# Kernel tuning notes

Hardware: AMD Instinct MI355X
Metric: run time of the kernel (lower is better)

The kernel has to match this reference:

```python
import jax, jax.numpy as jnp
import numpy as np

B, S, D, H = 32, 512, 512, 8  # note: source requires S == D due to swapped shape tuple in multi_head_attention
DK = D // H  # 64
FF = 200     # hard-coded FFN width in source
LN_EPS = 1e-5


def setup_inputs() -> dict:
    key = jax.random.key(0)
    ks = jax.random.split(key, 20)
    s = 0.02
    return {
        "x": jax.random.normal(ks[0], (B, S, D), dtype=jnp.float32),
        # per-head projections, stacked: torch Linear weight shape is [out, in] = [DK, D]
        "Wq": jax.random.normal(ks[1], (H, DK, D), dtype=jnp.float32) * s,
        "bq": jax.random.normal(ks[2], (H, DK), dtype=jnp.float32) * s,
        "Wk": jax.random.normal(ks[3], (H, DK, D), dtype=jnp.float32) * s,
        "bk": jax.random.normal(ks[4], (H, DK), dtype=jnp.float32) * s,
        "Wv": jax.random.normal(ks[5], (H, DK, D), dtype=jnp.float32) * s,
        "bv": jax.random.normal(ks[6], (H, DK), dtype=jnp.float32) * s,
        "Wo": jax.random.normal(ks[7], (D, D), dtype=jnp.float32) * s,
        "bo": jax.random.normal(ks[8], (D,), dtype=jnp.float32) * s,
        "W1": jax.random.normal(ks[9], (FF, D), dtype=jnp.float32) * s,
        "b1": jax.random.normal(ks[10], (FF,), dtype=jnp.float32) * s,
        "W2": jax.random.normal(ks[11], (FF, FF), dtype=jnp.float32) * s,
        "b2": jax.random.normal(ks[12], (FF,), dtype=jnp.float32) * s,
        "W3": jax.random.normal(ks[13], (D, FF), dtype=jnp.float32) * s,
        "b3": jax.random.normal(ks[14], (D,), dtype=jnp.float32) * s,
        # single SHARED LayerNorm over last two dims (S, D)
        "gamma": jnp.ones((S, D), dtype=jnp.float32),
        "beta": jnp.zeros((S, D), dtype=jnp.float32),
    }


def _layernorm2d(y, gamma, beta):
    # torch LayerNorm(normalized_shape=(S, D)): normalize over last two axes, biased variance
    m = jnp.mean(y, axis=(-2, -1), keepdims=True)
    v = jnp.mean(jnp.square(y - m), axis=(-2, -1), keepdims=True)
    return (y - m) * jax.lax.rsqrt(v + LN_EPS) * gamma + beta


def reference(x, Wq, bq, Wk, bk, Wv, bv, Wo, bo, W1, b1, W2, b2, W3, b3, gamma, beta):
    # --- multi-head attention (vectorized over the original per-head Python loop) ---
    q = jnp.einsum('bsd,hkd->bhsk', x, Wq) + bq[None, :, None, :]
    k = jnp.einsum('bsd,hkd->bhsk', x, Wk) + bk[None, :, None, :]
    v = jnp.einsum('bsd,hkd->bhsk', x, Wv) + bv[None, :, None, :]
    scores = jnp.einsum('bhsk,bhtk->bhst', q, k) / jnp.sqrt(jnp.float32(DK))
    attn = jax.nn.softmax(scores, axis=-1)
    heads = jnp.einsum('bhst,bhtk->bhsk', attn, v)          # [B,H,S,DK]
    concat = heads.transpose(0, 2, 1, 3).reshape(B, S, D)    # concat heads along feature dim
    y = jnp.einsum('bsd,ed->bse', concat, Wo) + bo + x       # output proj + residual
    # --- post-attention LayerNorm (shared params) ---
    y = _layernorm2d(y, gamma, beta)
    # --- feed-forward: D -> 200 -> 200 -> D, residual, LayerNorm (same shared LN) ---
    f = jax.nn.relu(jnp.einsum('bsd,fd->bsf', y, W1) + b1)
    f = jax.nn.relu(jnp.einsum('bsf,gf->bsg', f, W2) + b2)
    f = jnp.einsum('bsf,df->bsd', f, W3) + b3
    y = _layernorm2d(f + y, gamma, beta)
    # --- final LayerNorm (same shared LN again) ---
    return _layernorm2d(y, gamma, beta)
```

## Files before the change

kernel.cpp:

```cpp
#include <hip/hip_runtime.h>
#include <hip/hip_bf16.h>
#include <stdint.h>

#define B_  32
#define S_  512
#define D_  512
#define H_  8
#define DK_ 64
#define FF_ 200
#define FFP 256
#define M_  (B_*S_)
#define MSD ((size_t)B_*S_*D_)

typedef __hip_bfloat16 bf16;
typedef __attribute__((ext_vector_type(8))) short short8;
typedef __attribute__((ext_vector_type(4))) float f32x4;
typedef __attribute__((ext_vector_type(4))) unsigned short us4;

__device__ inline float b2f(bf16 v) { return __bfloat162float(v); }
__device__ inline bf16  f2b(float v){ return __float2bfloat16(v); }
__device__ inline unsigned short f2bu(float v) {
  union { bf16 h; unsigned short u; } cv; cv.h = __float2bfloat16(v); return cv.u;
}
__device__ __forceinline__ void async16(const bf16* g, bf16* l) {
  __builtin_amdgcn_global_load_lds((const __attribute__((address_space(1))) void*)g,
                                   (__attribute__((address_space(3))) void*)l, 16, 0, 0);
}

__global__ void detect_kernel(const unsigned short* __restrict__ xu, int* __restrict__ flag) {
  __shared__ int mx[256];
  const int tid = threadIdx.x;
  int m = 0;
  for (int i = tid * 2; i < 8192; i += 512) {
    int e = (xu[i] >> 7) & 0xFF;
    m = m > e ? m : e;
  }
  mx[tid] = m;
  __syncthreads();
  for (int st = 128; st; st >>= 1) {
    if (tid < st) mx[tid] = mx[tid] > mx[tid + st] ? mx[tid] : mx[tid + st];
    __syncthreads();
  }
  if (tid == 0) *flag = (mx[0] >= 0xC0) ? 1 : 0;
}

__global__ void zero_stats(float* stats) { if (threadIdx.x < 192) stats[threadIdx.x] = 0.f; }

__global__ __launch_bounds__(256) void cvt_x8(const void* __restrict__ in, bf16* __restrict__ out,
                                              const int* __restrict__ flag) {
  const bool f32in = (*flag != 0);
  size_t i = ((size_t)blockIdx.x * 256 + threadIdx.x) * 8;
  const size_t stride = (size_t)gridDim.x * 256 * 8;
  for (; i < MSD; i += stride) {
    if (f32in) {
      const float4 a = ((const float4*)in)[i/4];
      const float4 b = ((const float4*)in)[i/4 + 1];
      uint4 o; unsigned short* po = (unsigned short*)&o;
      po[0]=f2bu(a.x); po[1]=f2bu(a.y); po[2]=f2bu(a.z); po[3]=f2bu(a.w);
      po[4]=f2bu(b.x); po[5]=f2bu(b.y); po[6]=f2bu(b.z); po[7]=f2bu(b.w);
      *(uint4*)((unsigned short*)out + i) = o;
    } else {
      *(uint4*)((unsigned short*)out + i) = *(const uint4*)((const unsigned short*)in + i);
    }
  }
}

struct Seg { const void* src; void* dst; int srcRows, srcK, dstK, total; };
struct Segs { Seg s[16]; unsigned int isbf; };

__global__ __launch_bounds__(256) void cvt_all(Segs sg, const int* __restrict__ flag) {
  const bool f32in = (*flag != 0);
  const int seg = blockIdx.x & 15;
  const Seg sd = sg.s[seg];
  const int stride = (gridDim.x >> 4) * 256;
  const bool nopad = (sd.srcK == sd.dstK);
  for (int i = (blockIdx.x >> 4) * 256 + threadIdx.x; i < sd.total; i += stride) {
    int sidx; bool valid;
    if (nopad) { sidx = i; valid = (i < sd.srcRows * sd.srcK); }
    else {
      int r = i / sd.dstK, c = i - r * sd.dstK;
      valid = (r < sd.srcRows) && (c < sd.srcK);
      sidx = r * sd.srcK + c;
    }
    float v = 0.f;
    if (valid) v = f32in ? ((const float*)sd.src)[sidx] : b2f(((const bf16*)sd.src)[sidx]);
    if (sg.isbf & (1u << seg)) ((unsigned short*)sd.dst)[i] = f2bu(v);
    else                       ((float*)sd.dst)[i] = v;
  }
}

template<int MODE, int STATS, typename OUT>
__global__ __launch_bounds__(256) void gemm_mfma(
    const bf16* __restrict__ A, const bf16* __restrict__ W, const float* __restrict__ bias,
    const bf16* __restrict__ R, OUT* __restrict__ C, int M, int N, int K,
    float* __restrict__ stats)
{
  __shared__ bf16 As[128 * 32];
  __shared__ bf16 Bs[128 * 32];
  const int tid  = threadIdx.x;
  const int bm   = blockIdx.x * 128;
  const int bn   = blockIdx.y * 128;
  const int w    = tid >> 6;
  const int lane = tid & 63;
  const int qd   = lane >> 4;
  const int ln   = lane & 15;
  const int wr   = (w >> 1) * 64;
  const int wc   = (w & 1) * 64;

  const int r0 = lane >> 2;
  const int ch = (lane & 3) * 8;
  const bf16* Ag0 = A + (size_t)(bm + w*16 + r0) * K + ch;
  const bf16* Ag1 = Ag0 + (size_t)64 * K;
  const bf16* Bg0 = W + (size_t)(bn + w*16 + r0) * K + ch;
  const bf16* Bg1 = Bg0 + (size_t)64 * K;
  bf16* Al0 = As + w*512 + lane*8;
  bf16* Al1 = Al0 + 2048;
  bf16* Bl0 = Bs + w*512 + lane*8;
  bf16* Bl1 = Bl0 + 2048;

  f32x4 acc[4][4] = {};

  for (int k0 = 0; k0 < K; k0 += 32) {
    async16(Ag0 + k0, Al0);
    async16(Ag1 + k0, Al1);
    async16(Bg0 + k0, Bl0);
    async16(Bg1 + k0, Bl1);
    __syncthreads();

    short8 af[4], bfr[4];
#pragma unroll
    for (int i = 0; i < 4; i++) af[i]  = *(const short8*)(As + (wr + i*16 + ln)*32 + qd*8);
#pragma unroll
    for (int j = 0; j < 4; j++) bfr[j] = *(const short8*)(Bs + (wc + j*16 + ln)*32 + qd*8);
#pragma unroll
    for (int i = 0; i < 4; i++)
#pragma unroll
      for (int j = 0; j < 4; j++)
        acc[i][j] = __builtin_amdgcn_mfma_f32_16x16x32_bf16(af[i], bfr[j], acc[i][j], 0, 0, 0);
    __syncthreads();
  }

  float s_acc = 0.f, ss_acc = 0.f;
#pragma unroll
  for (int i = 0; i < 4; i++) {
#pragma unroll
    for (int j = 0; j < 4; j++) {
      int n = bn + wc + j*16 + ln;
      float bval = bias[n];
#pragma unroll
      for (int rg = 0; rg < 4; rg++) {
        int m = bm + wr + i*16 + qd*4 + rg;
        float val = acc[i][j][rg] + bval;
        if (MODE == 1) val = fmaxf(val, 0.f);
        if (MODE == 2) val += b2f(R[(size_t)m * N + n]);
        if (STATS) { s_acc += val; ss_acc += val * val; }
        if (MODE == 5) {
          int b = m >> 9, s = m & 511, t = n >> 9, nn = n & 511;
          int h = nn >> 6, dk = nn & 63;
          bf16* Cb = (bf16*)C;
          if (t == 2) Cb[2*MSD + ((size_t)((b*H_ + h)*DK_ + dk))*S_ + s] = f2b(val);
          else        Cb[(size_t)t*MSD + ((size_t)((b*H_ + h)*S_ + s))*DK_ + dk] = f2b(val);
        } else {
          if (sizeof(OUT) == 4) ((float*)C)[(size_t)m * N + n] = val;
          else                  ((bf16*)C)[(size_t)m * N + n]  = f2b(val);
        }
      }
    }
  }

  if (STATS) {
    float* red = (float*)As;
    red[tid] = s_acc; red[256 + tid] = ss_acc;
    __syncthreads();
    for (int st = 128; st; st >>= 1) {
      if (tid < st) { red[tid] += red[tid + st]; red[256 + tid] += red[256 + tid + st]; }
      __syncthreads();
    }
    if (tid == 0) {
      int b = bm >> 9;
      atomicAdd(&stats[b*2],     red[0]);
      atomicAdd(&stats[b*2 + 1], red[256]);
    }
  }
}

__global__ __launch_bounds__(1024, 4) void attn_lds(const bf16* __restrict__ q,
    const bf16* __restrict__ k, const bf16* __restrict__ vT, bf16* __restrict__ cat)
{
  __shared__ bf16 Ks[2 * 512 * 32];
  __shared__ bf16 Vs[64 * 520];
  __shared__ bf16 pbuf[16][16][40];

  const int tid  = threadIdx.x;
  const int w    = tid >> 6;
  const int lane = tid & 63;
  const int qd   = lane >> 4;
  const int ln   = lane & 15;
  const int bh   = blockIdx.x;
  const int b    = bh >> 3, h = bh & 7;

  const bf16* kbase = k  + (size_t)bh * S_ * DK_;
  const bf16* vbase = vT + (size_t)bh * DK_ * S_;

  for (int c = tid; c < 4096; c += 1024) {
    int part = c & 3, key = (c >> 2) & 511, ks = c >> 11;
    async16(kbase + key*64 + ks*32 + part*8, Ks + c*8);
  }
  {
    int j = tid & 63;
    for (int dk = tid >> 6; dk < 64; dk += 16) {
      uint4 v = *(const uint4*)(vbase + (size_t)dk*512 + j*8);
      *(uint4*)(Vs + dk*520 + j*8) = v;
    }
  }
  const bf16* qbase = q + (size_t)(bh*S_ + w*32) * DK_;
  short8 bq[2][2];
#pragma unroll
  for (int qt = 0; qt < 2; qt++)
#pragma unroll
    for (int ks = 0; ks < 2; ks++)
      bq[qt][ks] = *(const short8*)(qbase + (size_t)(qt*16 + ln)*DK_ + ks*32 + qd*8);

  __syncthreads();

  bf16 (*pb)[40] = pbuf[w];
  f32x4 o[2][4] = {};
  float l[2] = {0.f, 0.f};

  for (int st = 0; st < 16; st++) {
    short8 ak[2][2];
#pragma unroll
    for (int kt = 0; kt < 2; kt++)
#pragma unroll
      for (int ks = 0; ks < 2; ks++)
        ak[kt][ks] = *(const short8*)(Ks + ks*16384 + (st*32 + kt*16 + ln)*32 + qd*8);
    f32x4 s[2][2] = {};
#pragma unroll
    for (int kt = 0; kt < 2; kt++)
#pragma unroll
      for (int qt = 0; qt < 2; qt++) {
        s[kt][qt] = __builtin_amdgcn_mfma_f32_16x16x32_bf16(ak[kt][0], bq[qt][0], s[kt][qt], 0, 0, 0);
        s[kt][qt] = __builtin_amdgcn_mfma_f32_16x16x32_bf16(ak[kt][1], bq[qt][1], s[kt][qt], 0, 0, 0);
      }
    float e[2][2][4];
#pragma unroll
    for (int kt = 0; kt < 2; kt++)
#pragma unroll
      for (int qt = 0; qt < 2; qt++) {
#pragma unroll
        for (int rg = 0; rg < 4; rg++) {
          float ev = __expf(s[kt][qt][rg] * 0.125f);
          e[kt][qt][rg] = ev;
          l[qt] += ev;
        }
      }
#pragma unroll
    for (int qt = 0; qt < 2; qt++) {
#pragma unroll
      for (int kt = 0; kt < 2; kt++) {
        uint2 pk;
        pk.x = (unsigned)f2bu(e[kt][qt][0]) | ((unsigned)f2bu(e[kt][qt][1]) << 16);
        pk.y = (unsigned)f2bu(e[kt][qt][2]) | ((unsigned)f2bu(e[kt][qt][3]) << 16);
        *(uint2*)&pb[ln][kt*16 + qd*4] = pk;
      }
      short8 ap = *(const short8*)&pb[ln][qd*8];
#pragma unroll
      for (int nt = 0; nt < 4; nt++) {
        short8 bv = *(const short8*)(Vs + (nt*16 + ln)*520 + st*32 + qd*8);
        o[qt][nt] = __builtin_amdgcn_mfma_f32_16x16x32_bf16(ap, bv, o[qt][nt], 0, 0, 0);
      }
    }
  }

#pragma unroll
  for (int qt = 0; qt < 2; qt++) {
    l[qt] += __shfl_xor(l[qt], 16);
    l[qt] += __shfl_xor(l[qt], 32);
  }
  float inv0 = 1.f / l[0], inv1 = 1.f / l[1];

  const size_t crow0 = (size_t)(b*S_ + w*32) * D_ + h*DK_;
#pragma unroll
  for (int qt = 0; qt < 2; qt++) {
#pragma unroll
    for (int rg = 0; rg < 4; rg++) {
      float ivv = __shfl(qt ? inv1 : inv0, qd*4 + rg);
      int r = qt*16 + qd*4 + rg;
      bf16* cp = cat + crow0 + (size_t)r * D_ + ln;
#pragma unroll
      for (int nt = 0; nt < 4; nt++) cp[nt*16] = f2b(o[qt][nt][rg] * ivv);
    }
  }
}

__global__ __launch_bounds__(256) void ln_apply_bf16(const float* __restrict__ in,
    const float* __restrict__ stats, const float* __restrict__ gamma,
    const float* __restrict__ beta, bf16* __restrict__ out)
{
  const int b = blockIdx.x >> 4;
  const float invN = 1.f / (float)(S_*D_);
  const float m    = stats[b*2] * invN;
  const float var  = stats[b*2+1] * invN - m*m;
  const float rstd = rsqrtf(var + 1e-5f);
  size_t v = (size_t)b * 65536 + (blockIdx.x & 15) * 4096 + threadIdx.x;
#pragma unroll 4
  for (int it = 0; it < 16; it++, v += 256) {
    float4 x = ((const float4*)in)[v];
    size_t e = (v * 4) & (S_*D_ - 1);
    float4 g = *(const float4*)(gamma + e);
    float4 bt= *(const float4*)(beta + e);
    us4 o;
    o[0] = f2bu((x.x - m) * rstd * g.x + bt.x);
    o[1] = f2bu((x.y - m) * rstd * g.y + bt.y);
    o[2] = f2bu((x.z - m) * rstd * g.z + bt.z);
    o[3] = f2bu((x.w - m) * rstd * g.w + bt.w);
    *(us4*)((unsigned short*)out + v*4) = o;
  }
}

__global__ __launch_bounds__(256) void ln_apply_b16_stats(const float* __restrict__ in,
    const float* __restrict__ stats, const float* __restrict__ gamma,
    const float* __restrict__ beta, bf16* __restrict__ out, float* __restrict__ stats3)
{
  __shared__ float red[512];
  const int b = blockIdx.x >> 4;
  const float invN = 1.f / (float)(S_*D_);
  const float m    = stats[b*2] * invN;
  const float var  = stats[b*2+1] * invN - m*m;
  const float rstd = rsqrtf(var + 1e-5f);
  size_t v = (size_t)b * 65536 + (blockIdx.x & 15) * 4096 + threadIdx.x;
  float s_acc = 0.f, ss_acc = 0.f;
#pragma unroll 4
  for (int it = 0; it < 16; it++, v += 256) {
    float4 x = ((const float4*)in)[v];
    size_t e = (v * 4) & (S_*D_ - 1);
    float4 g = *(const float4*)(gamma + e);
    float4 bt= *(const float4*)(beta + e);
    us4 o;
    float o0 = (x.x - m) * rstd * g.x + bt.x;
    float o1 = (x.y - m) * rstd * g.y + bt.y;
    float o2 = (x.z - m) * rstd * g.z + bt.z;
    float o3 = (x.w - m) * rstd * g.w + bt.w;
    o[0] = f2bu(o0); o[1] = f2bu(o1); o[2] = f2bu(o2); o[3] = f2bu(o3);
    s_acc  += o0 + o1 + o2 + o3;
    ss_acc += o0*o0 + o1*o1 + o2*o2 + o3*o3;
    *(us4*)((unsigned short*)out + v*4) = o;
  }
  const int tid = threadIdx.x;
  red[tid] = s_acc; red[256 + tid] = ss_acc;
  __syncthreads();
  for (int st = 128; st; st >>= 1) {
    if (tid < st) { red[tid] += red[tid + st]; red[256 + tid] += red[256 + tid + st]; }
    __syncthreads();
  }
  if (tid == 0) {
    atomicAdd(&stats3[b*2],     red[0]);
    atomicAdd(&stats3[b*2 + 1], red[256]);
  }
}

__global__ __launch_bounds__(256) void ln_apply_out(const bf16* __restrict__ in,
    const float* __restrict__ stats, const float* __restrict__ gamma,
    const float* __restrict__ beta, void* __restrict__ out, const int* __restrict__ flag)
{
  const bool f32 = (*flag != 0);
  const int b = blockIdx.x >> 4;
  const float invN = 1.f / (float)(S_*D_);
  const float m    = stats[b*2] * invN;
  const float var  = stats[b*2+1] * invN - m*m;
  const float rstd = rsqrtf(var + 1e-5f);
  size_t v = (size_t)b * 65536 + (blockIdx.x & 15) * 4096 + threadIdx.x;
#pragma unroll 4
  for (int it = 0; it < 16; it++, v += 256) {
    us4 xi = *(const us4*)((const unsigned short*)in + v*4);
    union { unsigned short u; bf16 h; } c0{xi[0]}, c1{xi[1]}, c2{xi[2]}, c3{xi[3]};
    size_t e = (v * 4) & (S_*D_ - 1);
    float4 g = *(const float4*)(gamma + e);
    float4 bt= *(const float4*)(beta + e);
    float4 o;
    o.x = (b2f(c0.h) - m) * rstd * g.x + bt.x;
    o.y = (b2f(c1.h) - m) * rstd * g.y + bt.y;
    o.z = (b2f(c2.h) - m) * rstd * g.z + bt.z;
    o.w = (b2f(c3.h) - m) * rstd * g.w + bt.w;
    if (f32) ((float4*)out)[v] = o;
    else {
      us4 ob;
      ob[0] = f2bu(o.x); ob[1] = f2bu(o.y); ob[2] = f2bu(o.z); ob[3] = f2bu(o.w);
      *(us4*)((unsigned short*)out + v*4) = ob;
    }
  }
}

extern "C" void kernel_launch(void* const* d_in, const int* in_sizes, int n_in,
                              void* d_out, int out_size, void* d_ws, size_t ws_size,
                              hipStream_t stream)
{
  char* p = (char*)d_ws;
  auto alloc_b = [&](size_t elems) { void* r = p; p += elems * 2; return (bf16*)r; };
  auto alloc_f = [&](size_t elems) {
    p = (char*)(((uintptr_t)p + 15) & ~(uintptr_t)15); void* r = p; p += elems * 4; return (float*)r;
  };

  bf16* xb   = alloc_b(MSD);
  bf16* qkv  = alloc_b(3 * MSD);
  bf16* catb = alloc_b(MSD);
  bf16* wqkv = alloc_b(3 * 512 * 512);
  bf16* wo   = alloc_b(512 * 512);
  bf16* w1p  = alloc_b((size_t)FFP * 512);
  bf16* w2p  = alloc_b((size_t)FFP * FFP);
  bf16* w3p  = alloc_b((size_t)512 * FFP);
  float* yA  = alloc_f(MSD);
  float* yB  = alloc_f(MSD);
  float* bqkv= alloc_f(3 * 512);
  float* bo  = alloc_f(512);
  float* b1p = alloc_f(FFP);
  float* b2p = alloc_f(FFP);
  float* b3  = alloc_f(512);
  float* gm  = alloc_f((size_t)S_ * D_);
  float* bt  = alloc_f((size_t)S_ * D_);
  float* stats = alloc_f(192);
  int*   flag  = (int*)alloc_f(16);
  if ((size_t)(p - (char*)d_ws) > ws_size) return;

  bf16* qb   = qkv;
  bf16* kbuf = qkv + MSD;
  bf16* vTb  = qkv + 2 * MSD;
  bf16*  y1b = qb;
  bf16*  f1  = kbuf;
  bf16*  f2  = kbuf + (size_t)M_ * FFP;
  bf16*  y2b = vTb;
  float* st1 = stats, *st2 = stats + 64, *st3 = stats + 128;

  detect_kernel<<<1, 256, 0, stream>>>((const unsigned short*)d_in[0], flag);
  zero_stats<<<1, 256, 0, stream>>>(stats);
  cvt_x8<<<2048, 256, 0, stream>>>(d_in[0], xb, flag);

  Segs sg;
  sg.s[0]  = { d_in[1],  wqkv,               512, 512, 512, 512*512 };
  sg.s[1]  = { d_in[3],  wqkv + 512*512,     512, 512, 512, 512*512 };
  sg.s[2]  = { d_in[5],  wqkv + 2*512*512,   512, 512, 512, 512*512 };
  sg.s[3]  = { d_in[7],  wo,                 512, 512, 512, 512*512 };
  sg.s[4]  = { d_in[9],  w1p,                FF_, 512, 512, FFP*512 };
  sg.s[5]  = { d_in[11], w2p,                FF_, FF_, FFP, FFP*FFP };
  sg.s[6]  = { d_in[13], w3p,                512, FF_, FFP, 512*FFP };
  sg.s[7]  = { d_in[2],  bqkv,               1, 512, 512, 512 };
  sg.s[8]  = { d_in[4],  bqkv + 512,         1, 512, 512, 512 };
  sg.s[9]  = { d_in[6],  bqkv + 1024,        1, 512, 512, 512 };
  sg.s[10] = { d_in[8],  bo,                 1, 512, 512, 512 };
  sg.s[11] = { d_in[10], b1p,                1, FF_, FFP, FFP };
  sg.s[12] = { d_in[12], b2p,                1, FF_, FFP, FFP };
  sg.s[13] = { d_in[14], b3,                 1, 512, 512, 512 };
  sg.s[14] = { d_in[15], gm,                 1, S_*D_, S_*D_, S_*D_ };
  sg.s[15] = { d_in[16], bt,                 1, S_*D_, S_*D_, S_*D_ };
  sg.isbf = 0x007F;
  cvt_all<<<1024, 256, 0, stream>>>(sg, flag);

  dim3 blk(256);

  gemm_mfma<5, 0, bf16><<<dim3(M_/128, 12), blk, 0, stream>>>(
      xb, wqkv, bqkv, nullptr, qkv, M_, 1536, 512, nullptr);

  attn_lds<<<B_*H_, 1024, 0, stream>>>(qb, kbuf, vTb, catb);

  gemm_mfma<2, 1, float><<<dim3(M_/128, 4), blk, 0, stream>>>(
      catb, wo, bo, xb, yA, M_, 512, 512, st1);

  ln_apply_bf16<<<512, blk, 0, stream>>>(yA, st1, gm, bt, y1b);

  gemm_mfma<1, 0, bf16><<<dim3(M_/128, 2), blk, 0, stream>>>(
      y1b, w1p, b1p, nullptr, f1, M_, FFP, 512, nullptr);
  gemm_mfma<1, 0, bf16><<<dim3(M_/128, 2), blk, 0, stream>>>(
      f1, w2p, b2p, nullptr, f2, M_, FFP, FFP, nullptr);
  gemm_mfma<2, 1, float><<<dim3(M_/128, 4), blk, 0, stream>>>(
      f2, w3p, b3, y1b, yB, M_, 512, FFP, st2);

  ln_apply_b16_stats<<<512, blk, 0, stream>>>(yB, st2, gm, bt, y2b, st3);
  ln_apply_out<<<512, blk, 0, stream>>>(y2b, st3, gm, bt, d_out, flag);
}
```

Baseline: 321.8 us.

## Store QKV row-major, transpose V in LDS, keep pre-LN activations in bf16

The QKV GEMM now writes a plain row-major [M,1536] bf16 tensor instead of scattering into per-head Q/K and a transposed V layout. The attention kernel reads K, Q and V straight from that interleaved buffer and transposes V into LDS with scalar stores. The output-projection and FFN3 GEMMs now emit bf16 instead of fp32 pre-LayerNorm activations, which halves that traffic and lets the fp32 workspace buffers go. It also folds zero_stats into detect_kernel to save a launch. The risks are bank conflicts from the scalar LDS transposes and lower precision in the LayerNorm inputs.

```diff
diff --git a/kernel.cpp b/kernel.cpp
--- a/kernel.cpp
+++ b/kernel.cpp
@@ -11,6 +11,7 @@
 #define FFP 256
 #define M_  (B_*S_)
 #define MSD ((size_t)B_*S_*D_)
+#define NQKV 1536
 
 typedef __hip_bfloat16 bf16;
 typedef __attribute__((ext_vector_type(8))) short short8;
@@ -22,14 +23,19 @@
 __device__ inline unsigned short f2bu(float v) {
   union { bf16 h; unsigned short u; } cv; cv.h = __float2bfloat16(v); return cv.u;
 }
+__device__ inline float bu2f(unsigned short u) {
+  union { unsigned short u; bf16 h; } cv; cv.u = u; return b2f(cv.h);
+}
 __device__ __forceinline__ void async16(const bf16* g, bf16* l) {
   __builtin_amdgcn_global_load_lds((const __attribute__((address_space(1))) void*)g,
                                    (__attribute__((address_space(3))) void*)l, 16, 0, 0);
 }
 
-__global__ void detect_kernel(const unsigned short* __restrict__ xu, int* __restrict__ flag) {
+__global__ void detect_kernel(const unsigned short* __restrict__ xu, int* __restrict__ flag,
+                              float* __restrict__ stats) {
   __shared__ int mx[256];
   const int tid = threadIdx.x;
+  if (tid < 192) stats[tid] = 0.f;
   int m = 0;
   for (int i = tid * 2; i < 8192; i += 512) {
     int e = (xu[i] >> 7) & 0xFF;
@@ -43,8 +49,6 @@
   }
   if (tid == 0) *flag = (mx[0] >= 0xC0) ? 1 : 0;
 }
-
-__global__ void zero_stats(float* stats) { if (threadIdx.x < 192) stats[threadIdx.x] = 0.f; }
 
 __global__ __launch_bounds__(256) void cvt_x8(const void* __restrict__ in, bf16* __restrict__ out,
                                               const int* __restrict__ flag) {
@@ -154,16 +158,8 @@
         if (MODE == 1) val = fmaxf(val, 0.f);
         if (MODE == 2) val += b2f(R[(size_t)m * N + n]);
         if (STATS) { s_acc += val; ss_acc += val * val; }
-        if (MODE == 5) {
-          int b = m >> 9, s = m & 511, t = n >> 9, nn = n & 511;
-          int h = nn >> 6, dk = nn & 63;
-          bf16* Cb = (bf16*)C;
-          if (t == 2) Cb[2*MSD + ((size_t)((b*H_ + h)*DK_ + dk))*S_ + s] = f2b(val);
-          else        Cb[(size_t)t*MSD + ((size_t)((b*H_ + h)*S_ + s))*DK_ + dk] = f2b(val);
-        } else {
-          if (sizeof(OUT) == 4) ((float*)C)[(size_t)m * N + n] = val;
-          else                  ((bf16*)C)[(size_t)m * N + n]  = f2b(val);
-        }
+        if (sizeof(OUT) == 4) ((float*)C)[(size_t)m * N + n] = val;
+        else                  ((bf16*)C)[(size_t)m * N + n]  = f2b(val);
       }
     }
   }
@@ -184,8 +180,8 @@
   }
 }
 
-__global__ __launch_bounds__(1024, 4) void attn_lds(const bf16* __restrict__ q,
-    const bf16* __restrict__ k, const bf16* __restrict__ vT, bf16* __restrict__ cat)
+__global__ __launch_bounds__(1024, 4) void attn_lds(const bf16* __restrict__ qkv,
+                                                    bf16* __restrict__ cat)
 {
   __shared__ bf16 Ks[2 * 512 * 32];
   __shared__ bf16 Vs[64 * 520];
@@ -198,28 +194,26 @@
   const int ln   = lane & 15;
   const int bh   = blockIdx.x;
   const int b    = bh >> 3, h = bh & 7;
-
-  const bf16* kbase = k  + (size_t)bh * S_ * DK_;
-  const bf16* vbase = vT + (size_t)bh * DK_ * S_;
+  const bf16* base = qkv + (size_t)b * 512 * NQKV + h * 64;
 
   for (int c = tid; c < 4096; c += 1024) {
     int part = c & 3, key = (c >> 2) & 511, ks = c >> 11;
-    async16(kbase + key*64 + ks*32 + part*8, Ks + c*8);
-  }
-  {
-    int j = tid & 63;
-    for (int dk = tid >> 6; dk < 64; dk += 16) {
-      uint4 v = *(const uint4*)(vbase + (size_t)dk*512 + j*8);
-      *(uint4*)(Vs + dk*520 + j*8) = v;
-    }
-  }
-  const bf16* qbase = q + (size_t)(bh*S_ + w*32) * DK_;
+    async16(base + (size_t)key * NQKV + 512 + ks*32 + part*8, Ks + c*8);
+  }
+  for (int c = tid; c < 4096; c += 1024) {
+    int dkg = c & 7, key = c >> 3;
+    uint4 vv = *(const uint4*)(base + (size_t)key * NQKV + 1024 + dkg*8);
+    const unsigned short* pv = (const unsigned short*)&vv;
+#pragma unroll
+    for (int j = 0; j < 8; j++)
+      *(unsigned short*)&Vs[(dkg*8 + j)*520 + key] = pv[j];
+  }
   short8 bq[2][2];
 #pragma unroll
   for (int qt = 0; qt < 2; qt++)
 #pragma unroll
     for (int ks = 0; ks < 2; ks++)
-      bq[qt][ks] = *(const short8*)(qbase + (size_t)(qt*16 + ln)*DK_ + ks*32 + qd*8);
+      bq[qt][ks] = *(const short8*)(base + (size_t)(w*32 + qt*16 + ln) * NQKV + ks*32 + qd*8);
 
   __syncthreads();
 
@@ -246,14 +240,13 @@
 #pragma unroll
     for (int kt = 0; kt < 2; kt++)
 #pragma unroll
-      for (int qt = 0; qt < 2; qt++) {
+      for (int qt = 0; qt < 2; qt++)
 #pragma unroll
         for (int rg = 0; rg < 4; rg++) {
           float ev = __expf(s[kt][qt][rg] * 0.125f);
           e[kt][qt][rg] = ev;
           l[qt] += ev;
         }
-      }
 #pragma unroll
     for (int qt = 0; qt < 2; qt++) {
 #pragma unroll
@@ -293,7 +286,7 @@
   }
 }
 
-__global__ __launch_bounds__(256) void ln_apply_bf16(const float* __restrict__ in,
+__global__ __launch_bounds__(256) void ln_b16_b16(const bf16* __restrict__ in,
     const float* __restrict__ stats, const float* __restrict__ gamma,
     const float* __restrict__ beta, bf16* __restrict__ out)
 {
@@ -305,20 +298,20 @@
   size_t v = (size_t)b * 65536 + (blockIdx.x & 15) * 4096 + threadIdx.x;
 #pragma unroll 4
   for (int it = 0; it < 16; it++, v += 256) {
-    float4 x = ((const float4*)in)[v];
+    us4 xi = *(const us4*)((const unsigned short*)in + v*4);
     size_t e = (v * 4) & (S_*D_ - 1);
     float4 g = *(const float4*)(gamma + e);
     float4 bt= *(const float4*)(beta + e);
     us4 o;
-    o[0] = f2bu((x.x - m) * rstd * g.x + bt.x);
-    o[1] = f2bu((x.y - m) * rstd * g.y + bt.y);
-    o[2] = f2bu((x.z - m) * rstd * g.z + bt.z);
-    o[3] = f2bu((x.w - m) * rstd * g.w + bt.w);
+    o[0] = f2bu((bu2f(xi[0]) - m) * rstd * g.x + bt.x);
+    o[1] = f2bu((bu2f(xi[1]) - m) * rstd * g.y + bt.y);
+    o[2] = f2bu((bu2f(xi[2]) - m) * rstd * g.z + bt.z);
+    o[3] = f2bu((bu2f(xi[3]) - m) * rstd * g.w + bt.w);
     *(us4*)((unsigned short*)out + v*4) = o;
   }
 }
 
-__global__ __launch_bounds__(256) void ln_apply_b16_stats(const float* __restrict__ in,
+__global__ __launch_bounds__(256) void ln_b16_b16_stats(const bf16* __restrict__ in,
     const float* __restrict__ stats, const float* __restrict__ gamma,
     const float* __restrict__ beta, bf16* __restrict__ out, float* __restrict__ stats3)
 {
@@ -332,15 +325,15 @@
   float s_acc = 0.f, ss_acc = 0.f;
 #pragma unroll 4
   for (int it = 0; it < 16; it++, v += 256) {
-    float4 x = ((const float4*)in)[v];
+    us4 xi = *(const us4*)((const unsigned short*)in + v*4);
     size_t e = (v * 4) & (S_*D_ - 1);
     float4 g = *(const float4*)(gamma + e);
     float4 bt= *(const float4*)(beta + e);
+    float o0 = (bu2f(xi[0]) - m) * rstd * g.x + bt.x;
+    float o1 = (bu2f(xi[1]) - m) * rstd * g.y + bt.y;
+    float o2 = (bu2f(xi[2]) - m) * rstd * g.z + bt.z;
+    float o3 = (bu2f(xi[3]) - m) * rstd * g.w + bt.w;
     us4 o;
-    float o0 = (x.x - m) * rstd * g.x + bt.x;
-    float o1 = (x.y - m) * rstd * g.y + bt.y;
-    float o2 = (x.z - m) * rstd * g.z + bt.z;
-    float o3 = (x.w - m) * rstd * g.w + bt.w;
     o[0] = f2bu(o0); o[1] = f2bu(o1); o[2] = f2bu(o2); o[3] = f2bu(o3);
     s_acc  += o0 + o1 + o2 + o3;
     ss_acc += o0*o0 + o1*o1 + o2*o2 + o3*o3;
@@ -373,15 +366,14 @@
 #pragma unroll 4
   for (int it = 0; it < 16; it++, v += 256) {
     us4 xi = *(const us4*)((const unsigned short*)in + v*4);
-    union { unsigned short u; bf16 h; } c0{xi[0]}, c1{xi[1]}, c2{xi[2]}, c3{xi[3]};
     size_t e = (v * 4) & (S_*D_ - 1);
     float4 g = *(const float4*)(gamma + e);
     float4 bt= *(const float4*)(beta + e);
     float4 o;
-    o.x = (b2f(c0.h) - m) * rstd * g.x + bt.x;
-    o.y = (b2f(c1.h) - m) * rstd * g.y + bt.y;
-    o.z = (b2f(c2.h) - m) * rstd * g.z + bt.z;
-    o.w = (b2f(c3.h) - m) * rstd * g.w + bt.w;
+    o.x = (bu2f(xi[0]) - m) * rstd * g.x + bt.x;
+    o.y = (bu2f(xi[1]) - m) * rstd * g.y + bt.y;
+    o.z = (bu2f(xi[2]) - m) * rstd * g.z + bt.z;
+    o.w = (bu2f(xi[3]) - m) * rstd * g.w + bt.w;
     if (f32) ((float4*)out)[v] = o;
     else {
       us4 ob;
@@ -409,8 +401,6 @@
   bf16* w1p  = alloc_b((size_t)FFP * 512);
   bf16* w2p  = alloc_b((size_t)FFP * FFP);
   bf16* w3p  = alloc_b((size_t)512 * FFP);
-  float* yA  = alloc_f(MSD);
-  float* yB  = alloc_f(MSD);
   float* bqkv= alloc_f(3 * 512);
   float* bo  = alloc_f(512);
   float* b1p = alloc_f(FFP);
@@ -422,17 +412,15 @@
   int*   flag  = (int*)alloc_f(16);
   if ((size_t)(p - (char*)d_ws) > ws_size) return;
 
-  bf16* qb   = qkv;
-  bf16* kbuf = qkv + MSD;
-  bf16* vTb  = qkv + 2 * MSD;
-  bf16*  y1b = qb;
-  bf16*  f1  = kbuf;
-  bf16*  f2  = kbuf + (size_t)M_ * FFP;
-  bf16*  y2b = vTb;
+  bf16* y1b = qkv;
+  bf16* f1  = qkv + MSD;
+  bf16* f2  = qkv + MSD + (size_t)M_ * FFP;
+  bf16* yA  = qkv + 2 * MSD;
+  bf16* yB  = catb;
+  bf16* y2b = yA;
   float* st1 = stats, *st2 = stats + 64, *st3 = stats + 128;
 
-  detect_kernel<<<1, 256, 0, stream>>>((const unsigned short*)d_in[0], flag);
-  zero_stats<<<1, 256, 0, stream>>>(stats);
+  detect_kernel<<<1, 256, 0, stream>>>((const unsigned short*)d_in[0], flag, stats);
   cvt_x8<<<2048, 256, 0, stream>>>(d_in[0], xb, flag);
 
   Segs sg;
@@ -457,23 +445,23 @@
 
   dim3 blk(256);
 
-  gemm_mfma<5, 0, bf16><<<dim3(M_/128, 12), blk, 0, stream>>>(
-      xb, wqkv, bqkv, nullptr, qkv, M_, 1536, 512, nullptr);
-
-  attn_lds<<<B_*H_, 1024, 0, stream>>>(qb, kbuf, vTb, catb);
-
-  gemm_mfma<2, 1, float><<<dim3(M_/128, 4), blk, 0, stream>>>(
+  gemm_mfma<0, 0, bf16><<<dim3(M_/128, NQKV/128), blk, 0, stream>>>(
+      xb, wqkv, bqkv, nullptr, qkv, M_, NQKV, 512, nullptr);
+
+  attn_lds<<<B_*H_, 1024, 0, stream>>>(qkv, catb);
+
+  gemm_mfma<2, 1, bf16><<<dim3(M_/128, 4), blk, 0, stream>>>(
       catb, wo, bo, xb, yA, M_, 512, 512, st1);
 
-  ln_apply_bf16<<<512, blk, 0, stream>>>(yA, st1, gm, bt, y1b);
+  ln_b16_b16<<<512, blk, 0, stream>>>(yA, st1, gm, bt, y1b);
 
   gemm_mfma<1, 0, bf16><<<dim3(M_/128, 2), blk, 0, stream>>>(
       y1b, w1p, b1p, nullptr, f1, M_, FFP, 512, nullptr);
   gemm_mfma<1, 0, bf16><<<dim3(M_/128, 2), blk, 0, stream>>>(
       f1, w2p, b2p, nullptr, f2, M_, FFP, FFP, nullptr);
-  gemm_mfma<2, 1, float><<<dim3(M_/128, 4), blk, 0, stream>>>(
+  gemm_mfma<2, 1, bf16><<<dim3(M_/128, 4), blk, 0, stream>>>(
       f2, w3p, b3, y1b, yB, M_, 512, FFP, st2);
 
-  ln_apply_b16_stats<<<512, blk, 0, stream>>>(yB, st2, gm, bt, y2b, st3);
+  ln_b16_b16_stats<<<512, blk, 0, stream>>>(yB, st2, gm, bt, y2b, st3);
   ln_apply_out<<<512, blk, 0, stream>>>(y2b, st3, gm, bt, d_out, flag);
 }
```

Result: faster. 299.9 us (-6.8%).
